# Performance work log

Measured on AMD Instinct MI355X. Metric: run time of the kernel, lower is better.

Reference implementation:

```python
import jax, jax.numpy as jnp
import numpy as np

H, W = 3000, 3000

def setup_inputs() -> dict:
    rng = np.random.default_rng(0)
    activities_np = rng.random((H, W)) < 0.9
    nb_active = int(activities_np.sum())
    vertex_weights = jnp.asarray(rng.random((H, W), dtype=np.float32))
    neighbors = jnp.array([(1, 0), (-1, 0), (0, 1), (0, -1)], dtype=jnp.int32)  # rook contiguity
    return {
        "activities": jnp.asarray(activities_np),
        "vertex_weights": vertex_weights,
        "neighbors": neighbors,
        "nb_active": nb_active,
    }


def reference(activities, vertex_weights, neighbors, nb_active):
    nrows, ncols = activities.shape
    num_nodes = nb_active  # static python int
    # active vertex index -> (i, j) coords, row-major order (matches jnp.nonzero)
    rows, cols = jnp.nonzero(activities, size=num_nodes)
    source_xy = jnp.stack([rows, cols], axis=1)  # [N, 2]
    # (i, j) -> active vertex index map, -1 for inactive
    active_map = jnp.full((nrows, ncols), -1, dtype=jnp.int32)
    active_map = active_map.at[rows, cols].set(jnp.arange(num_nodes, dtype=jnp.int32))
    # candidate neighbor coordinates [N, K, 2]
    cand = source_xy[:, None, :] + neighbors[None, :, :].astype(source_xy.dtype)
    ci_raw, cj_raw = cand[..., 0], cand[..., 1]
    in_bounds = (ci_raw >= 0) & (ci_raw < nrows) & (cj_raw >= 0) & (cj_raw < ncols)
    ci = jnp.clip(ci_raw, 0, nrows - 1)
    cj = jnp.clip(cj_raw, 0, ncols - 1)
    target_active = activities[ci, cj]
    valid = in_bounds & target_active  # [N, K]
    # zero out invalid coords before gather (matches original)
    vi = jnp.where(valid, ci_raw, 0)
    vj = jnp.where(valid, cj_raw, 0)
    tgt = jnp.where(valid, active_map[vi, vj], 0)
    src = jnp.where(valid, jnp.arange(num_nodes, dtype=jnp.int32)[:, None], 0)
    vals = jnp.where(valid, vertex_weights[vi, vj], 0.0)
    indices = jnp.stack([src.ravel(), tgt.ravel()], axis=1)  # [N*K, 2]
    return vals.ravel(), indices  # BCOO data and indices, shape (num_nodes, num_nodes)
```

## Files before the change

kernel.cpp:

```cpp
#include <hip/hip_runtime.h>
#include <cstdint>

#define HH 3000
#define WW 3000
#define WPR 48
#define NW (HH * WPR)

typedef unsigned long long u64;
typedef float f4v __attribute__((ext_vector_type(4)));

#define BITS_OFF 0
#define ROWS_OFF 1152000
#define P_OFF    1164032

__device__ __forceinline__ void nt_store4(const float4& v, float4* p) {
    f4v x; x.x = v.x; x.y = v.y; x.z = v.z; x.w = v.w;
    __builtin_nontemporal_store(x, (f4v*)p);
}

__device__ __forceinline__ int detect_mode(const void* acts, int t, int lane, int wv,
                                           int* s_red, int* s_mode) {
    int v = (int)((const unsigned*)acts)[t];
    #pragma unroll
    for (int off = 32; off > 0; off >>= 1) v = max(v, __shfl_down(v, off));
    if (lane == 0) s_red[wv] = v;
    __syncthreads();
    if (t == 0) {
        int mx = max(max(s_red[0], s_red[1]), max(s_red[2], s_red[3]));
        *s_mode = (mx > 1 && mx <= 0x01010101) ? 1 : 0;
    }
    __syncthreads();
    return *s_mode;
}

__global__ __launch_bounds__(256) void k_build(const void* __restrict__ acts,
                                               u64* __restrict__ bits,
                                               int* __restrict__ rowSums) {
    __shared__ int s_red[4];
    __shared__ int s_mode;
    const int t = threadIdx.x, lane = t & 63, wv = t >> 6;
    const int mode = detect_mode(acts, t, lane, wv, s_red, &s_mode);

    const int r = blockIdx.x;
    const long rowbase = (long)r * WW;
    int mycnt = 0;
    for (int it = 0; it < 12; ++it) {
        int wi = it * 4 + wv;
        int j = wi * 64 + lane;
        bool a = false;
        if (j < WW) {
            if (mode) a = ((const unsigned char*)acts)[rowbase + j] != 0;
            else      a = ((const unsigned*)acts)[rowbase + j] != 0u;
        }
        u64 m = __ballot(a);
        if (lane == 0) {
            bits[r * WPR + wi] = m;
            mycnt += __popcll(m);
        }
    }
    if (lane == 0) s_red[wv] = mycnt;
    __syncthreads();
    if (t == 0) rowSums[r] = s_red[0] + s_red[1] + s_red[2] + s_red[3];
}

__global__ __launch_bounds__(256) void k_prefixP(const u64* __restrict__ bits,
                                                 const int* __restrict__ rowSums,
                                                 int* __restrict__ P) {
    __shared__ int s_red[4];
    const int t = threadIdx.x, lane = t & 63, wv = t >> 6;
    const int r0 = blockIdx.x * 4;
    int s = 0;
    for (int idx = t; idx < r0; idx += 256) s += rowSums[idx];
    #pragma unroll
    for (int off = 32; off > 0; off >>= 1) s += __shfl_down(s, off);
    if (lane == 0) s_red[wv] = s;
    __syncthreads();
    int base = s_red[0] + s_red[1] + s_red[2] + s_red[3];

    const int r = r0 + wv;
    if (r < HH) {
        int rbase = base;
        if (wv >= 1) rbase += rowSums[r0];
        if (wv >= 2) rbase += rowSums[r0 + 1];
        if (wv >= 3) rbase += rowSums[r0 + 2];
        const int w = r * WPR + lane;
        int v = (lane < WPR) ? __popcll(bits[w]) : 0;
        int x = v;
        #pragma unroll
        for (int off = 1; off < 64; off <<= 1) {
            int y = __shfl_up(x, off);
            if (lane >= off) x += y;
        }
        if (lane < WPR) P[w] = rbase + (x - v);
    }
}

__global__ __launch_bounds__(256) void k_emit(const u64* __restrict__ bits,
                                              const int* __restrict__ P,
                                              const float* __restrict__ wts,
                                              float* __restrict__ out, int N) {
    const int t = threadIdx.x;
    const int lane = t & 63;
    const int wv = t >> 6;
    const int i = blockIdx.y;
    const int j0 = blockIdx.x * 256 + t;

    __shared__ float4 s_vals[4][64];
    __shared__ float4 s_inds[4][128];

    bool inrow = (j0 < WW);
    int j = inrow ? j0 : (WW - 1);
    int wi = j >> 6, bit = j & 63;
    int w = i * WPR + wi;
    u64 mself = bits[w];
    bool cellact = (mself >> bit) & 1ull;
    int v = P[w] + __popcll(mself & ((1ull << bit) - 1ull));
    bool act = inrow && cellact;
    if (!inrow && cellact) v += 1;

    int n0 = __shfl(v, 0);
    int a  = __shfl(v + (act ? 1 : 0), 63) - n0;

    if (act) {
        float nf = (float)v;
        const long c = (long)i * WW + j;
        float val[4], sf[4], tf[4];
        {
            bool ok = (i < HH - 1);
            u64 wd = ok ? bits[w + WPR] : 0ull;
            bool aa = ok && ((wd >> bit) & 1ull);
            val[0] = aa ? wts[c + WW] : 0.f; sf[0] = aa ? nf : 0.f;
            tf[0] = aa ? (float)(P[w + WPR] + __popcll(wd & ((1ull << bit) - 1ull))) : 0.f;
        }
        {
            bool ok = (i > 0);
            u64 wd = ok ? bits[w - WPR] : 0ull;
            bool aa = ok && ((wd >> bit) & 1ull);
            val[1] = aa ? wts[c - WW] : 0.f; sf[1] = aa ? nf : 0.f;
            tf[1] = aa ? (float)(P[w - WPR] + __popcll(wd & ((1ull << bit) - 1ull))) : 0.f;
        }
        {
            bool ok = (j < WW - 1);
            int wn = (bit < 63) ? w : w + 1;
            int b2 = (bit < 63) ? bit + 1 : 0;
            u64 wd = ok ? ((bit < 63) ? mself : bits[wn]) : 0ull;
            bool aa = ok && ((wd >> b2) & 1ull);
            val[2] = aa ? wts[c + 1] : 0.f; sf[2] = aa ? nf : 0.f;
            tf[2] = aa ? (float)(P[wn] + __popcll(wd & ((1ull << b2) - 1ull))) : 0.f;
        }
        {
            bool ok = (j > 0);
            int wn = (bit > 0) ? w : w - 1;
            int b2 = (bit > 0) ? bit - 1 : 63;
            u64 wd = ok ? ((bit > 0) ? mself : bits[wn]) : 0ull;
            bool aa = ok && ((wd >> b2) & 1ull);
            val[3] = aa ? wts[c - 1] : 0.f; sf[3] = aa ? nf : 0.f;
            tf[3] = aa ? (float)(P[wn] + __popcll(wd & ((1ull << b2) - 1ull))) : 0.f;
        }
        int rloc = v - n0;
        s_vals[wv][rloc]         = make_float4(val[0], val[1], val[2], val[3]);
        s_inds[wv][2 * rloc]     = make_float4(sf[0], tf[0], sf[1], tf[1]);
        s_inds[wv][2 * rloc + 1] = make_float4(sf[2], tf[2], sf[3], tf[3]);
    }
    float4* valsg = (float4*)out;
    float4* indsg = (float4*)(out + (size_t)N * 4);
    if (lane < a) nt_store4(s_vals[wv][lane], &valsg[(size_t)n0 + lane]);
    int twoa = 2 * a;
    if (lane < twoa)      nt_store4(s_inds[wv][lane],      &indsg[2 * (size_t)n0 + lane]);
    if (lane + 64 < twoa) nt_store4(s_inds[wv][lane + 64], &indsg[2 * (size_t)n0 + 64 + lane]);
}

extern "C" void kernel_launch(void* const* d_in, const int* in_sizes, int n_in,
                              void* d_out, int out_size, void* d_ws, size_t ws_size,
                              hipStream_t stream) {
    const void* acts = d_in[0];
    const float* wts = (const float*)d_in[1];
    float* out = (float*)d_out;
    const int N = out_size / 12;

    u64* bits = (u64*)((char*)d_ws + BITS_OFF);
    int* rows = (int*)((char*)d_ws + ROWS_OFF);
    int* P    = (int*)((char*)d_ws + P_OFF);

    k_build<<<HH, 256, 0, stream>>>(acts, bits, rows);
    k_prefixP<<<(HH + 3) / 4, 256, 0, stream>>>(bits, rows, P);
    k_emit<<<dim3(12, HH), 256, 0, stream>>>(bits, P, wts, out, N);
}
```

Measured before the change: 107.8 us.

## Drop LDS staging in emit kernel and process two words per wave

The emit kernel no longer compacts results through shared memory. Each active lane now writes its three float4 records straight to global memory at its prefix index. Each wave also handles two 64-bit mask words, so the grid is halved. This removes LDS traffic and the shuffles used for compaction, but global stores become non-contiguous wherever inactive cells leave gaps, which may hurt write coalescing.

```diff
diff --git a/kernel.cpp b/kernel.cpp
--- a/kernel.cpp
+++ b/kernel.cpp
@@ -13,8 +13,8 @@
 #define ROWS_OFF 1152000
 #define P_OFF    1164032
 
-__device__ __forceinline__ void nt_store4(const float4& v, float4* p) {
-    f4v x; x.x = v.x; x.y = v.y; x.z = v.z; x.w = v.w;
+__device__ __forceinline__ void nt_store4(float a, float b, float c, float d, float4* p) {
+    f4v x; x.x = a; x.y = b; x.z = c; x.w = d;
     __builtin_nontemporal_store(x, (f4v*)p);
 }
 
@@ -103,71 +103,60 @@
     const int lane = t & 63;
     const int wv = t >> 6;
     const int i = blockIdx.y;
-    const int j0 = blockIdx.x * 256 + t;
 
-    __shared__ float4 s_vals[4][64];
-    __shared__ float4 s_inds[4][128];
+    float4* valsg = (float4*)out;
+    float4* indsg = (float4*)(out + (size_t)N * 4);
 
-    bool inrow = (j0 < WW);
-    int j = inrow ? j0 : (WW - 1);
-    int wi = j >> 6, bit = j & 63;
-    int w = i * WPR + wi;
-    u64 mself = bits[w];
-    bool cellact = (mself >> bit) & 1ull;
-    int v = P[w] + __popcll(mself & ((1ull << bit) - 1ull));
-    bool act = inrow && cellact;
-    if (!inrow && cellact) v += 1;
+    #pragma unroll
+    for (int half = 0; half < 2; ++half) {
+        const int wi = blockIdx.x * 8 + half * 4 + wv;
+        const int j = wi * 64 + lane;
+        const int w = i * WPR + wi;
+        const u64 mself = bits[w];
+        if (!((mself >> lane) & 1ull)) continue;
 
-    int n0 = __shfl(v, 0);
-    int a  = __shfl(v + (act ? 1 : 0), 63) - n0;
+        const int v = P[w] + __popcll(mself & ((1ull << lane) - 1ull));
+        const float nf = (float)v;
+        const long c = (long)i * WW + j;
 
-    if (act) {
-        float nf = (float)v;
-        const long c = (long)i * WW + j;
-        float val[4], sf[4], tf[4];
+        float val0, val1, val2, val3, sf0, sf1, sf2, sf3, tf0, tf1, tf2, tf3;
         {
             bool ok = (i < HH - 1);
             u64 wd = ok ? bits[w + WPR] : 0ull;
-            bool aa = ok && ((wd >> bit) & 1ull);
-            val[0] = aa ? wts[c + WW] : 0.f; sf[0] = aa ? nf : 0.f;
-            tf[0] = aa ? (float)(P[w + WPR] + __popcll(wd & ((1ull << bit) - 1ull))) : 0.f;
+            bool aa = ok && ((wd >> lane) & 1ull);
+            val0 = aa ? wts[c + WW] : 0.f; sf0 = aa ? nf : 0.f;
+            tf0 = aa ? (float)(P[w + WPR] + __popcll(wd & ((1ull << lane) - 1ull))) : 0.f;
         }
         {
             bool ok = (i > 0);
             u64 wd = ok ? bits[w - WPR] : 0ull;
-            bool aa = ok && ((wd >> bit) & 1ull);
-            val[1] = aa ? wts[c - WW] : 0.f; sf[1] = aa ? nf : 0.f;
-            tf[1] = aa ? (float)(P[w - WPR] + __popcll(wd & ((1ull << bit) - 1ull))) : 0.f;
+            bool aa = ok && ((wd >> lane) & 1ull);
+            val1 = aa ? wts[c - WW] : 0.f; sf1 = aa ? nf : 0.f;
+            tf1 = aa ? (float)(P[w - WPR] + __popcll(wd & ((1ull << lane) - 1ull))) : 0.f;
         }
         {
             bool ok = (j < WW - 1);
-            int wn = (bit < 63) ? w : w + 1;
-            int b2 = (bit < 63) ? bit + 1 : 0;
-            u64 wd = ok ? ((bit < 63) ? mself : bits[wn]) : 0ull;
+            int wn = (lane < 63) ? w : w + 1;
+            int b2 = (lane < 63) ? lane + 1 : 0;
+            u64 wd = ok ? ((lane < 63) ? mself : bits[wn]) : 0ull;
             bool aa = ok && ((wd >> b2) & 1ull);
-            val[2] = aa ? wts[c + 1] : 0.f; sf[2] = aa ? nf : 0.f;
-            tf[2] = aa ? (float)(P[wn] + __popcll(wd & ((1ull << b2) - 1ull))) : 0.f;
+            val2 = aa ? wts[c + 1] : 0.f; sf2 = aa ? nf : 0.f;
+            tf2 = aa ? (float)(P[wn] + __popcll(wd & ((1ull << b2) - 1ull))) : 0.f;
         }
         {
             bool ok = (j > 0);
-            int wn = (bit > 0) ? w : w - 1;
-            int b2 = (bit > 0) ? bit - 1 : 63;
-            u64 wd = ok ? ((bit > 0) ? mself : bits[wn]) : 0ull;
+            int wn = (lane > 0) ? w : w - 1;
+            int b2 = (lane > 0) ? lane - 1 : 63;
+            u64 wd = ok ? ((lane > 0) ? mself : bits[wn]) : 0ull;
             bool aa = ok && ((wd >> b2) & 1ull);
-            val[3] = aa ? wts[c - 1] : 0.f; sf[3] = aa ? nf : 0.f;
-            tf[3] = aa ? (float)(P[wn] + __popcll(wd & ((1ull << b2) - 1ull))) : 0.f;
+            val3 = aa ? wts[c - 1] : 0.f; sf3 = aa ? nf : 0.f;
+            tf3 = aa ? (float)(P[wn] + __popcll(wd & ((1ull << b2) - 1ull))) : 0.f;
         }
-        int rloc = v - n0;
-        s_vals[wv][rloc]         = make_float4(val[0], val[1], val[2], val[3]);
-        s_inds[wv][2 * rloc]     = make_float4(sf[0], tf[0], sf[1], tf[1]);
-        s_inds[wv][2 * rloc + 1] = make_float4(sf[2], tf[2], sf[3], tf[3]);
+
+        nt_store4(val0, val1, val2, val3, &valsg[v]);
+        nt_store4(sf0, tf0, sf1, tf1, &indsg[2 * (size_t)v]);
+        nt_store4(sf2, tf2, sf3, tf3, &indsg[2 * (size_t)v + 1]);
     }
-    float4* valsg = (float4*)out;
-    float4* indsg = (float4*)(out + (size_t)N * 4);
-    if (lane < a) nt_store4(s_vals[wv][lane], &valsg[(size_t)n0 + lane]);
-    int twoa = 2 * a;
-    if (lane < twoa)      nt_store4(s_inds[wv][lane],      &indsg[2 * (size_t)n0 + lane]);
-    if (lane + 64 < twoa) nt_store4(s_inds[wv][lane + 64], &indsg[2 * (size_t)n0 + 64 + lane]);
 }
 
 extern "C" void kernel_launch(void* const* d_in, const int* in_sizes, int n_in,
@@ -184,5 +173,5 @@
 
     k_build<<<HH, 256, 0, stream>>>(acts, bits, rows);
     k_prefixP<<<(HH + 3) / 4, 256, 0, stream>>>(bits, rows, P);
-    k_emit<<<dim3(12, HH), 256, 0, stream>>>(bits, P, wts, out, N);
+    k_emit<<<dim3(6, HH), 256, 0, stream>>>(bits, P, wts, out, N);
 }
```

Measured after the change: 108.8 us. No clear change (+0.9%).
